# Performance work log

Measured on AMD Instinct MI355X. Metric: run time of the kernel, lower is better.

The kernel has to match this reference:

```python
import jax, jax.numpy as jnp
import numpy as np

B, S, C, D, H = 2, 2048, 512, 768, 12
DH = D // H
DFF = 3072
EPS = 1e-5
NEG = 10000.0


def _layernorm(x, g, b):
    mu = jnp.mean(x, axis=-1, keepdims=True)
    var = jnp.mean((x - mu) ** 2, axis=-1, keepdims=True)
    return (x - mu) / jnp.sqrt(var + EPS) * g + b


def setup_inputs() -> dict:
    key = jax.random.key(0)
    ks = jax.random.split(key, 8)
    std = 0.02
    return {
        "x": jax.random.normal(ks[0], (B, S, D), jnp.float32),
        "context_seq": jax.random.normal(ks[1], (B, C, D), jnp.float32),
        "ln1_g": jnp.ones((D,), jnp.float32),
        "ln1_b": jnp.zeros((D,), jnp.float32),
        "Wattn": std * jax.random.normal(ks[2], (D, 3 * D), jnp.float32),
        "battn": jnp.zeros((3 * D,), jnp.float32),
        "Wref": std * jax.random.normal(ks[3], (D, 2 * D), jnp.float32),
        "bref": jnp.zeros((2 * D,), jnp.float32),
        "Wproj": std * jax.random.normal(ks[4], (D, D), jnp.float32),
        "bproj": jnp.zeros((D,), jnp.float32),
        "ln2_g": jnp.ones((D,), jnp.float32),
        "ln2_b": jnp.zeros((D,), jnp.float32),
        "W1": std * jax.random.normal(ks[5], (D, DFF), jnp.float32),
        "b1": jnp.zeros((DFF,), jnp.float32),
        "W2": std * jax.random.normal(ks[6], (DFF, D), jnp.float32),
        "b2": jnp.zeros((D,), jnp.float32),
        "context_attn_bias": jnp.ones((), jnp.float32),
        "cs_self_attn_mask_prob": 1,
    }


def reference(x, context_seq, ln1_g, ln1_b, Wattn, battn, Wref, bref,
              Wproj, bproj, ln2_g, ln2_b, W1, b1, W2, b2,
              context_attn_bias, cs_self_attn_mask_prob):
    # --- CoconBlock: no history_seq -> history_seq_len = 0, offset = 0 ---
    h1 = _layernorm(x, ln1_g, ln1_b)

    # fused qkv (Conv1D == x @ W + b)
    qkv = h1 @ Wattn + battn
    q, k, v = jnp.split(qkv, 3, axis=-1)            # each [B,S,D]
    kv_ctx = context_seq @ Wref + bref
    kc, vc = jnp.split(kv_ctx, 2, axis=-1)          # each [B,C,D]

    kp = jnp.concatenate([kc, k], axis=1)           # [B,C+S,D]
    vp = jnp.concatenate([vc, v], axis=1)
    ns = C + S

    qh = q.reshape(B, S, H, DH)
    kh = kp.reshape(B, ns, H, DH)
    vh = vp.reshape(B, ns, H, DH)

    # scores (scale=False in original call path -> unscaled QK^T)
    w = jnp.einsum('bqhd,bkhd->bhqk', qh, kh)       # [B,H,S,ns]

    qi = jnp.arange(S)[:, None]
    kj = jnp.arange(ns)[None, :]
    # causal bias slice: tril rows ns-nd..ns-1 -> attend iff kj <= qi + C
    causal = (kj <= qi + C).astype(w.dtype)
    w = w * causal - NEG * (1.0 - causal)

    # self-token mask (cs_self_attn_mask_prob == 1: fully deterministic path;
    # history_seq_len = 0 -> offset 0 -> masks element (i, i))
    if cs_self_attn_mask_prob > 0:
        stm = (kj != qi).astype(w.dtype)
        w = w * stm - NEG * (1.0 - stm)

    # context attention bias on the first C key columns
    ctx_cols = (kj < C).astype(w.dtype)
    w = w + context_attn_bias * ctx_cols

    p = jax.nn.softmax(w, axis=-1)                  # attn_dropout: eval/identity
    a = jnp.einsum('bhqk,bkhd->bqhd', p, vh).reshape(B, S, D)
    a = a @ Wproj + bproj                           # resid_dropout: identity

    x1 = x + a                                      # history_seq_len <= 1: no slice
    h2 = _layernorm(x1, ln2_g, ln2_b)
    m = jax.nn.silu(h2 @ W1 + b1) @ W2 + b2
    out = x1 + m
    return out[:, 1:, :]                            # include_sos_output=False
```

## Files before the change

### kernel.cpp

```cpp
#include <hip/hip_runtime.h>
#include <hip/hip_bf16.h>
#include <math.h>

#define B_   2
#define S_   2048
#define C_   512
#define D_   768
#define H_   12
#define DH_  64
#define DFF_ 3072
#define NS_  (C_ + S_)

typedef __attribute__((ext_vector_type(8))) short          bf16x8;
typedef __attribute__((ext_vector_type(4))) float          f32x4;
typedef __attribute__((ext_vector_type(8))) unsigned short us8;
typedef __attribute__((ext_vector_type(4))) unsigned short us4;

static __device__ __forceinline__ unsigned short f2b(float f) {
    unsigned int u = __float_as_uint(f);
    unsigned int r = (u + 0x7FFFu + ((u >> 16) & 1u)) >> 16;
    return (unsigned short)r;
}
static __device__ __forceinline__ float b2f(unsigned short u) {
    return __uint_as_float(((unsigned int)u) << 16);
}

#define ASYNC_LDS16(gp, lp)                                                     \
    __builtin_amdgcn_global_load_lds(                                           \
        (const __attribute__((address_space(1))) void*)(gp),                    \
        (__attribute__((address_space(3))) void*)(lp), 16, 0, 0)

#define XCD_SWIZZLE_2D(MB, NB, TM, TN)                                          \
    int nwg_ = gridDim.x * gridDim.y;                                           \
    int bid_ = blockIdx.y * gridDim.x + blockIdx.x;                             \
    int q8_  = nwg_ >> 3;                                                       \
    int swz_ = (bid_ & 7) * q8_ + (bid_ >> 3);                                  \
    int MB = (swz_ / gridDim.x) * (TM);                                         \
    int NB = (swz_ % gridDim.x) * (TN);

__global__ __launch_bounds__(256) void ln_kernel(const float* __restrict__ in,
                                                 const float* __restrict__ g,
                                                 const float* __restrict__ bta,
                                                 unsigned short* __restrict__ out)
{
    int row = blockIdx.x;
    int tid = threadIdx.x;
    const float* x = in + (size_t)row * D_;
    float v0 = x[tid], v1 = x[tid + 256], v2 = x[tid + 512];
    float s  = v0 + v1 + v2;
    float s2 = v0 * v0 + v1 * v1 + v2 * v2;
#pragma unroll
    for (int off = 32; off >= 1; off >>= 1) {
        s  += __shfl_down(s,  off, 64);
        s2 += __shfl_down(s2, off, 64);
    }
    __shared__ float sh[8];
    int lane = tid & 63, wv = tid >> 6;
    if (lane == 0) { sh[wv] = s; sh[4 + wv] = s2; }
    __syncthreads();
    s  = sh[0] + sh[1] + sh[2] + sh[3];
    s2 = sh[4] + sh[5] + sh[6] + sh[7];
    float mu   = s * (1.0f / D_);
    float var  = s2 * (1.0f / D_) - mu * mu;
    float rstd = rsqrtf(var + 1e-5f);
    unsigned short* o = out + (size_t)row * D_;
    o[tid]       = f2b((v0 - mu) * rstd * g[tid]       + bta[tid]);
    o[tid + 256] = f2b((v1 - mu) * rstd * g[tid + 256] + bta[tid + 256]);
    o[tid + 512] = f2b((v2 - mu) * rstd * g[tid + 512] + bta[tid + 512]);
}

__global__ __launch_bounds__(256) void wprep(
    const float* __restrict__ Wattn, const float* __restrict__ Wref,
    const float* __restrict__ Wproj, const float* __restrict__ W1,
    const float* __restrict__ W2,    const float* __restrict__ ctx,
    unsigned short* __restrict__ wattnT, unsigned short* __restrict__ wrefT,
    unsigned short* __restrict__ wprojT, unsigned short* __restrict__ w1T,
    unsigned short* __restrict__ w2T,    unsigned short* __restrict__ ctxb)
{
    int bid = blockIdx.x;
    if (bid >= 8064) {
        int i = (bid - 8064) * 256 + threadIdx.x;
        float4 v = ((const float4*)ctx)[i];
        us4 o = { f2b(v.x), f2b(v.y), f2b(v.z), f2b(v.w) };
        ((us4*)ctxb)[i] = o;
        return;
    }
    const float* in; unsigned short* outp; int K, N, nt;
    if (bid < 1728)      {             in = Wattn; outp = wattnT; K = 768;  N = 2304; nt = 72; }
    else if (bid < 2880) { bid -= 1728; in = Wref;  outp = wrefT;  K = 768;  N = 1536; nt = 48; }
    else if (bid < 3456) { bid -= 2880; in = Wproj; outp = wprojT; K = 768;  N = 768;  nt = 24; }
    else if (bid < 5760) { bid -= 3456; in = W1;    outp = w1T;    K = 768;  N = 3072; nt = 96; }
    else                 { bid -= 5760; in = W2;    outp = w2T;    K = 3072; N = 768;  nt = 24; }
    int n0 = (bid % nt) * 32, k0 = (bid / nt) * 32;

    __shared__ float t[32][33];
    int tx = threadIdx.x & 31, ty = threadIdx.x >> 5;
#pragma unroll
    for (int i = 0; i < 32; i += 8)
        t[ty + i][tx] = in[(size_t)(k0 + ty + i) * N + n0 + tx];
    __syncthreads();
#pragma unroll
    for (int i = 0; i < 32; i += 8)
        outp[(size_t)(n0 + ty + i) * K + k0 + tx] = f2b(t[tx][ty + i]);
}

#define GEMM_EPI_ELEM()                                                         \
    {                                                                           \
        float v = accv[q] + bv;                                                 \
        if (ACT) v = v / (1.0f + __expf(-v));                                   \
        if (RESID) v += resid[(size_t)grow * N + gcol];                         \
        if (OUTBF) {                                                            \
            outb[(size_t)grow * N + gcol] = f2b(v);                             \
        } else if (SLICE) {                                                     \
            int bb = grow >> 11, ss = grow & 2047;                              \
            if (ss > 0)                                                         \
                outf[((size_t)(bb * 2047 + ss - 1)) * N + gcol] = v;            \
        } else {                                                                \
            outf[(size_t)grow * N + gcol] = v;                                  \
        }                                                                       \
    }

template <int ACT, int RESID, int SLICE, int OUTBF>
__global__ __launch_bounds__(256) void gemm_mfma(
    const unsigned short* __restrict__ A,
    const unsigned short* __restrict__ BT,
    const float* __restrict__ bias,
    const float* __restrict__ resid,
    float* __restrict__ outf,
    unsigned short* __restrict__ outb,
    int M, int N, int K)
{
    __shared__ unsigned short Als[128 * 64];
    __shared__ unsigned short Bls[128 * 64];

    int tid  = threadIdx.x;
    int lane = tid & 63, w = tid >> 6;
    XCD_SWIZZLE_2D(mb, nb, 128, 128)
    int wr = w >> 1, wc = w & 1;

    f32x4 acc[4][4];
#pragma unroll
    for (int m = 0; m < 4; ++m)
#pragma unroll
        for (int n = 0; n < 4; ++n)
            acc[m][n] = (f32x4){0.f, 0.f, 0.f, 0.f};

    int srow = w * 32 + (lane >> 3);
    int scol = (lane & 7) * 8;
    const unsigned short* abase = A  + (size_t)(mb + srow) * K + scol;
    const unsigned short* bbase = BT + (size_t)(nb + srow) * K + scol;

    int arow_l = wr * 64 + (lane & 15);
    int brow_l = wc * 64 + (lane & 15);
    int kfrag  = (lane >> 4) * 8;

    for (int kk = 0; kk < K; kk += 64) {
        __syncthreads();
#pragma unroll
        for (int i = 0; i < 4; ++i) {
            ASYNC_LDS16(abase + (size_t)(i * 8) * K + kk,
                        (char*)Als + (w * 32 + i * 8) * 128);
            ASYNC_LDS16(bbase + (size_t)(i * 8) * K + kk,
                        (char*)Bls + (w * 32 + i * 8) * 128);
        }
        __syncthreads();
#pragma unroll
        for (int ks = 0; ks < 64; ks += 32) {
            bf16x8 af[4], bq[4];
#pragma unroll
            for (int m = 0; m < 4; ++m)
                af[m] = *(const bf16x8*)&Als[(arow_l + m * 16) * 64 + ks + kfrag];
#pragma unroll
            for (int n = 0; n < 4; ++n)
                bq[n] = *(const bf16x8*)&Bls[(brow_l + n * 16) * 64 + ks + kfrag];
#pragma unroll
            for (int m = 0; m < 4; ++m)
#pragma unroll
                for (int n = 0; n < 4; ++n)
                    acc[m][n] = __builtin_amdgcn_mfma_f32_16x16x32_bf16(
                        af[m], bq[n], acc[m][n], 0, 0, 0);
        }
    }

#pragma unroll
    for (int m = 0; m < 4; ++m) {
        int grow0 = mb + wr * 64 + m * 16 + ((lane >> 4) << 2);
#pragma unroll
        for (int n = 0; n < 4; ++n) {
            int gcol = nb + wc * 64 + n * 16 + (lane & 15);
            float bv = bias[gcol];
#pragma unroll
            for (int q = 0; q < 4; ++q) {
                int grow = grow0 + q;
                float accv[4] = {acc[m][n][0], acc[m][n][1], acc[m][n][2], acc[m][n][3]};
                GEMM_EPI_ELEM()
            }
        }
    }
}

template <int ACT, int RESID, int SLICE, int OUTBF>
__global__ __launch_bounds__(256) void gemm_mfma64(
    const unsigned short* __restrict__ A,
    const unsigned short* __restrict__ BT,
    const float* __restrict__ bias,
    const float* __restrict__ resid,
    float* __restrict__ outf,
    unsigned short* __restrict__ outb,
    int M, int N, int K)
{
    __shared__ unsigned short Als[64 * 64];
    __shared__ unsigned short Bls[128 * 64];

    int tid  = threadIdx.x;
    int lane = tid & 63, w = tid >> 6;
    XCD_SWIZZLE_2D(mb, nb, 64, 128)

    f32x4 acc[4][2];
#pragma unroll
    for (int m = 0; m < 4; ++m)
#pragma unroll
        for (int n = 0; n < 2; ++n)
            acc[m][n] = (f32x4){0.f, 0.f, 0.f, 0.f};

    int srow = w * 8 + (lane >> 3);
    int scol = (lane & 7) * 8;
    const unsigned short* abase = A  + (size_t)(mb + srow) * K + scol;
    const unsigned short* bbase = BT + (size_t)(nb + srow) * K + scol;

    int arow_l = lane & 15;
    int brow_l = w * 32 + (lane & 15);
    int kfrag  = (lane >> 4) * 8;

    for (int kk = 0; kk < K; kk += 64) {
        __syncthreads();
#pragma unroll
        for (int i = 0; i < 2; ++i)
            ASYNC_LDS16(abase + (size_t)(i * 32) * K + kk,
                        (char*)Als + i * 4096 + w * 1024);
#pragma unroll
        for (int i = 0; i < 4; ++i)
            ASYNC_LDS16(bbase + (size_t)(i * 32) * K + kk,
                        (char*)Bls + i * 4096 + w * 1024);
        __syncthreads();
#pragma unroll
        for (int ks = 0; ks < 64; ks += 32) {
            bf16x8 af[4], bq[2];
#pragma unroll
            for (int m = 0; m < 4; ++m)
                af[m] = *(const bf16x8*)&Als[(arow_l + m * 16) * 64 + ks + kfrag];
#pragma unroll
            for (int n = 0; n < 2; ++n)
                bq[n] = *(const bf16x8*)&Bls[(brow_l + n * 16) * 64 + ks + kfrag];
#pragma unroll
            for (int m = 0; m < 4; ++m)
#pragma unroll
                for (int n = 0; n < 2; ++n)
                    acc[m][n] = __builtin_amdgcn_mfma_f32_16x16x32_bf16(
                        af[m], bq[n], acc[m][n], 0, 0, 0);
        }
    }

#pragma unroll
    for (int m = 0; m < 4; ++m) {
        int grow0 = mb + m * 16 + ((lane >> 4) << 2);
#pragma unroll
        for (int n = 0; n < 2; ++n) {
            int gcol = nb + w * 32 + n * 16 + (lane & 15);
            float bv = bias[gcol];
#pragma unroll
            for (int q = 0; q < 4; ++q) {
                int grow = grow0 + q;
                float accv[4] = {acc[m][n][0], acc[m][n][1], acc[m][n][2], acc[m][n][3]};
                GEMM_EPI_ELEM()
            }
        }
    }
}

__device__ const int ATT_QT[21] = {10,9,8,7,6,5,15,15,14, 4,14,13,13,12, 3,12,11,11, 2,1,0};
__device__ const int ATT_T0[21] = { 0,0,0,0,0,0, 0,10, 0, 0,10, 0, 9, 0, 0, 9, 0, 8, 0,0,0};
__device__ const int ATT_T1[21] = {15,14,13,12,11,10,10,20,10, 9,19, 9,18, 9, 8,17, 8,16, 7,6,5};

__global__ __launch_bounds__(512, 2) void attn_mfma(const unsigned short* __restrict__ qkv,
                                                    const unsigned short* __restrict__ kvctx,
                                                    const float* __restrict__ cabp,
                                                    const int* __restrict__ smpp,
                                                    unsigned short* __restrict__ aout,
                                                    float* __restrict__ Opart,
                                                    float* __restrict__ mlpart)
{
    __shared__ unsigned short Kls[128 * 64];
    __shared__ unsigned short Vt [64 * 136];
    __shared__ unsigned short Pls[128 * 136];

    int bid = blockIdx.x;
    int j = (bid < 256) ? bid : 503 - (bid - 256);
    int rank = j / 24, grp = j % 24;
    int h = grp % 12, b = grp / 12;
    int qt = ATT_QT[rank], t0 = ATT_T0[rank], t1 = ATT_T1[rank];
    bool split = (t1 - t0) < (qt + 5);
    int half = (t0 > 0) ? 1 : 0;

    int tid = threadIdx.x;
    int l = tid & 63, w = tid >> 6;
    int g = l >> 4, lc = l & 15;
    float cab = *cabp;
    int   smp = *smpp;
    int qbase = qt * 128;

    bf16x8 qf0, qf1;
    {
        const unsigned short* qp = qkv + ((size_t)(b * S_ + qbase + w * 16 + lc)) * (3 * D_)
                                       + h * DH_ + g * 8;
        qf0 = *(const bf16x8*)(qp);
        qf1 = *(const bf16x8*)(qp + 32);
    }

    f32x4 acc[4];
#pragma unroll
    for (int n = 0; n < 4; ++n) acc[n] = (f32x4){0.f, 0.f, 0.f, 0.f};
    float mrow[4], lrow[4];
#pragma unroll
    for (int e = 0; e < 4; ++e) { mrow[e] = -1e30f; lrow[e] = 0.f; }

    int colu = 8 * ((l & 7) ^ (l >> 3));
    int kvr  = tid >> 3;
    int d0   = (tid & 7) * 8;
    int dsw  = (tid & 7) << 3;
    int vtrow[8];
#pragma unroll
    for (int jj = 0; jj < 8; ++jj) vtrow[jj] = (d0 + jj) * 136;
    int vo0 = kvr ^ dsw, vo1 = (64 + kvr) ^ dsw;
    int ksw  = (lc & 7) << 3;
    int koff0 = (g * 8) ^ ksw, koff1 = (32 + g * 8) ^ ksw;
    us8 vr0, vr1;

#define STAGE_TILE(TT)                                                                   \
    {                                                                                    \
        int kb2 = (TT) * 128;                                                            \
        bool isctx = (kb2 < C_);                                                         \
        _Pragma("unroll")                                                                \
        for (int s2 = 0; s2 < 2; ++s2) {                                                 \
            int s = w * 2 + s2;                                                          \
            int kj = kb2 + s * 8 + (l >> 3);                                             \
            const unsigned short* src = isctx                                            \
                ? kvctx + ((size_t)(b * C_ + kj)) * (2 * D_) + h * DH_ + colu            \
                : qkv + ((size_t)(b * S_ + kj - C_)) * (3 * D_) + D_ + h * DH_ + colu;   \
            ASYNC_LDS16(src, (char*)Kls + s * 1024);                                     \
        }                                                                                \
        int kv0 = kb2 + kvr;                                                             \
        vr0 = *(const us8*)(isctx                                                        \
            ? kvctx + ((size_t)(b * C_ + kv0)) * (2 * D_) + D_ + h * DH_ + d0            \
            : qkv + ((size_t)(b * S_ + kv0 - C_)) * (3 * D_) + 2 * D_ + h * DH_ + d0);   \
        vr1 = *(const us8*)(isctx                                                        \
            ? kvctx + ((size_t)(b * C_ + kv0 + 64)) * (2 * D_) + D_ + h * DH_ + d0       \
            : qkv + ((size_t)(b * S_ + kv0 + 64 - C_)) * (3 * D_) + 2 * D_ + h * DH_ + d0); \
    }

    STAGE_TILE(t0)

    for (int t = t0; t < t1; ++t) {
        int kb = t * 128;
        __syncthreads();

#pragma unroll
        for (int jj = 0; jj < 8; ++jj) {
            Vt[vtrow[jj] + vo0] = vr0[jj];
            Vt[vtrow[jj] + vo1] = vr1[jj];
        }

        f32x4 s4[8];
#pragma unroll
        for (int nf = 0; nf < 8; ++nf) s4[nf] = (f32x4){0.f, 0.f, 0.f, 0.f};
        __builtin_amdgcn_s_setprio(1);
#pragma unroll
        for (int nf = 0; nf < 8; ++nf) {
            bf16x8 kf0 = *(const bf16x8*)&Kls[(nf * 16 + lc) * 64 + koff0];
            bf16x8 kf1 = *(const bf16x8*)&Kls[(nf * 16 + lc) * 64 + koff1];
            s4[nf] = __builtin_amdgcn_mfma_f32_16x16x32_bf16(qf0, kf0, s4[nf], 0, 0, 0);
            s4[nf] = __builtin_amdgcn_mfma_f32_16x16x32_bf16(qf1, kf1, s4[nf], 0, 0, 0);
        }
        __builtin_amdgcn_s_setprio(0);

        bool edge_t = (t == qt + 4);
        bool diag_t = (kb == qbase) && (smp > 0);
        float tb = (kb < C_) ? cab : 0.0f;

        if (edge_t) {
#pragma unroll
            for (int nf = 0; nf < 8; ++nf) {
                int kj = kb + nf * 16 + lc;
#pragma unroll
                for (int e = 0; e < 4; ++e) {
                    int qi = qbase + w * 16 + g * 4 + e;
                    s4[nf][e] = (kj <= qi + C_) ? s4[nf][e] : -10000.0f;
                }
            }
        }
        if (diag_t) {
#pragma unroll
            for (int nf = 0; nf < 8; ++nf) {
                int kj = kb + nf * 16 + lc;
#pragma unroll
                for (int e = 0; e < 4; ++e) {
                    int qi = qbase + w * 16 + g * 4 + e;
                    if (kj == qi) s4[nf][e] = -10000.0f;
                }
            }
        }

        float tmax[4], mbase[4], psum[4];
#pragma unroll
        for (int e = 0; e < 4; ++e) {
            float u0 = fmaxf(fmaxf(s4[0][e], s4[1][e]), fmaxf(s4[2][e], s4[3][e]));
            float u1 = fmaxf(fmaxf(s4[4][e], s4[5][e]), fmaxf(s4[6][e], s4[7][e]));
            tmax[e] = fmaxf(u0, u1);
        }
#pragma unroll
        for (int e = 0; e < 4; ++e) {
            tmax[e] = fmaxf(tmax[e], __shfl_xor(tmax[e], 1));
            tmax[e] = fmaxf(tmax[e], __shfl_xor(tmax[e], 2));
            tmax[e] = fmaxf(tmax[e], __shfl_xor(tmax[e], 4));
            tmax[e] = fmaxf(tmax[e], __shfl_xor(tmax[e], 8));
        }
#pragma unroll
        for (int e = 0; e < 4; ++e) {
            float mn = fmaxf(mrow[e], tmax[e] + tb);
            if (mn > mrow[e]) {
                float sc = __expf(mrow[e] - mn);
#pragma unroll
                for (int nf2 = 0; nf2 < 4; ++nf2) acc[nf2][e] *= sc;
                lrow[e] *= sc;
                mrow[e] = mn;
            }
            mbase[e] = mrow[e] - tb;
            psum[e] = 0.f;
        }
#pragma unroll
        for (int nf = 0; nf < 8; ++nf)
#pragma unroll
            for (int e = 0; e < 4; ++e) {
                float p = __expf(s4[nf][e] - mbase[e]);
                s4[nf][e] = p;
                psum[e] += p;
            }
#pragma unroll
        for (int e = 0; e < 4; ++e) lrow[e] += psum[e];

#pragma unroll
        for (int e = 0; e < 4; ++e) {
            int q = w * 16 + g * 4 + e;
            int qrow = q * 136, qsw = (q & 7) << 3;
#pragma unroll
            for (int a = 0; a < 4; ++a) {
                unsigned int pk;
                asm("v_cvt_pk_bf16_f32 %0, %1, %2"
                    : "=v"(pk) : "v"(s4[2 * a][e]), "v"(s4[2 * a + 1][e]));
                int xk = (a * 32 + lc) ^ qsw;
                Pls[qrow + xk]        = (unsigned short)pk;
                Pls[qrow + (xk ^ 16)] = (unsigned short)(pk >> 16);
            }
        }

        __syncthreads();

        if (t + 1 < t1) STAGE_TILE(t + 1)

        {
            int qa = w * 16 + lc;
            int qrow = qa * 136, qsw = (qa & 7) << 3;
            __builtin_amdgcn_s_setprio(1);
#pragma unroll
            for (int ks2 = 0; ks2 < 4; ++ks2) {
                bf16x8 pf = *(const bf16x8*)&Pls[qrow + ((ks2 * 32 + g * 8) ^ qsw)];
#pragma unroll
                for (int nf2 = 0; nf2 < 4; ++nf2) {
                    int d = nf2 * 16 + lc;
                    bf16x8 vf = *(const bf16x8*)&Vt[d * 136 +
                                   ((ks2 * 32 + g * 8) ^ (((d >> 3) & 7) << 3))];
                    acc[nf2] = __builtin_amdgcn_mfma_f32_16x16x32_bf16(pf, vf, acc[nf2], 0, 0, 0);
                }
            }
            __builtin_amdgcn_s_setprio(0);
        }
    }

#pragma unroll
    for (int e = 0; e < 4; ++e) {
        lrow[e] += __shfl_xor(lrow[e], 1);
        lrow[e] += __shfl_xor(lrow[e], 2);
        lrow[e] += __shfl_xor(lrow[e], 4);
        lrow[e] += __shfl_xor(lrow[e], 8);
    }
    if (!split) {
#pragma unroll
        for (int e = 0; e < 4; ++e) {
            int q = qbase + w * 16 + g * 4 + e;
            float inv = 1.0f / lrow[e];
            unsigned short* dst = &aout[((size_t)(b * S_ + q)) * D_ + h * DH_];
#pragma unroll
            for (int nf2 = 0; nf2 < 4; ++nf2)
                dst[nf2 * 16 + lc] = f2b(acc[nf2][e] * inv);
        }
    } else {
        int rec = ((b * 12 + h) * 5 + (qt - 11)) * 2 + half;
        float* Ob  = Opart + (size_t)rec * 8192;
        float* mlb = mlpart + rec * 256;
#pragma unroll
        for (int e = 0; e < 4; ++e) {
            int row = w * 16 + g * 4 + e;
#pragma unroll
            for (int nf2 = 0; nf2 < 4; ++nf2)
                Ob[row * 64 + nf2 * 16 + lc] = acc[nf2][e];
            if (lc == 0) { mlb[row * 2] = mrow[e]; mlb[row * 2 + 1] = lrow[e]; }
        }
    }
#undef STAGE_TILE
}

__global__ __launch_bounds__(256) void attn_merge(const float* __restrict__ Opart,
                                                  const float* __restrict__ mlpart,
                                                  unsigned short* __restrict__ aout)
{
    int rec = blockIdx.x;
    int qidx = rec % 5;
    int bh = rec / 5;
    int h = bh % 12, b = bh / 12;
    int qt = 11 + qidx;
    int row = threadIdx.x >> 1, dbase = (threadIdx.x & 1) * 32;

    const float* O0  = Opart + ((size_t)(rec * 2 + 0)) * 8192 + row * 64 + dbase;
    const float* O1  = Opart + ((size_t)(rec * 2 + 1)) * 8192 + row * 64 + dbase;
    const float* ml0 = mlpart + (rec * 2 + 0) * 256 + row * 2;
    const float* ml1 = mlpart + (rec * 2 + 1) * 256 + row * 2;
    float m0 = ml0[0], l0 = ml0[1];
    float m1 = ml1[0], l1 = ml1[1];
    float m  = fmaxf(m0, m1);
    float c0 = __expf(m0 - m), c1 = __expf(m1 - m);
    float inv = 1.0f / (l0 * c0 + l1 * c1);

    int q = qt * 128 + row;
    unsigned short* dst = &aout[((size_t)(b * S_ + q)) * D_ + h * DH_ + dbase];
#pragma unroll
    for (int jj = 0; jj < 32; ++jj)
        dst[jj] = f2b((O0[jj] * c0 + O1[jj] * c1) * inv);
}

extern "C" void kernel_launch(void* const* d_in, const int* in_sizes, int n_in,
                              void* d_out, int out_size, void* d_ws, size_t ws_size,
                              hipStream_t stream)
{
    const float* x     = (const float*)d_in[0];
    const float* ctx   = (const float*)d_in[1];
    const float* ln1g  = (const float*)d_in[2];
    const float* ln1b  = (const float*)d_in[3];
    const float* Wattn = (const float*)d_in[4];
    const float* battn = (const float*)d_in[5];
    const float* Wref  = (const float*)d_in[6];
    const float* bref  = (const float*)d_in[7];
    const float* Wproj = (const float*)d_in[8];
    const float* bproj = (const float*)d_in[9];
    const float* ln2g  = (const float*)d_in[10];
    const float* ln2b  = (const float*)d_in[11];
    const float* W1    = (const float*)d_in[12];
    const float* b1    = (const float*)d_in[13];
    const float* W2    = (const float*)d_in[14];
    const float* b2    = (const float*)d_in[15];
    const float* cab   = (const float*)d_in[16];
    const int*   smp   = (const int*)d_in[17];
    float* out = (float*)d_out;

    float* ws = (float*)d_ws;
    unsigned short* qkvb   = (unsigned short*)(ws + 0);
    unsigned short* ff1b   = (unsigned short*)(ws + 0);
    unsigned short* kvctxb = (unsigned short*)(ws + 4718592);
    unsigned short* attnb  = (unsigned short*)(ws + 5505024);
    unsigned short* hb     = (unsigned short*)(ws + 7077888);
    float*          x1     = ws + 8650752;
    float*          Opart  = ws + 7077888;
    float*          mlpart = ws + 11010048;
    unsigned short* ctxb   = (unsigned short*)(ws + 11796480);
    unsigned short* wts    = (unsigned short*)(ws + 12189696);
    unsigned short* wattnT = wts;
    unsigned short* wrefT  = wts + 1769472;
    unsigned short* wprojT = wts + 2949120;
    unsigned short* w1T    = wts + 3538944;
    unsigned short* w2T    = wts + 5898240;

    wprep<<<8832, 256, 0, stream>>>(Wattn, Wref, Wproj, W1, W2, ctx,
                                    wattnT, wrefT, wprojT, w1T, w2T, ctxb);

    ln_kernel<<<B_ * S_, 256, 0, stream>>>(x, ln1g, ln1b, hb);
    gemm_mfma<0, 0, 0, 1><<<dim3(18, 32), 256, 0, stream>>>(
        hb, wattnT, battn, nullptr, nullptr, qkvb, 4096, 2304, 768);
    gemm_mfma64<0, 0, 0, 1><<<dim3(12, 16), 256, 0, stream>>>(
        ctxb, wrefT, bref, nullptr, nullptr, kvctxb, 1024, 1536, 768);
    attn_mfma<<<504, 512, 0, stream>>>(qkvb, kvctxb, cab, smp, attnb, Opart, mlpart);
    attn_merge<<<120, 256, 0, stream>>>(Opart, mlpart, attnb);
    gemm_mfma64<0, 1, 0, 0><<<dim3(6, 64), 256, 0, stream>>>(
        attnb, wprojT, bproj, x, x1, nullptr, 4096, 768, 768);
    ln_kernel<<<B_ * S_, 256, 0, stream>>>(x1, ln2g, ln2b, hb);
    gemm_mfma<1, 0, 0, 1><<<dim3(24, 32), 256, 0, stream>>>(
        hb, w1T, b1, nullptr, nullptr, ff1b, 4096, 3072, 768);
    gemm_mfma64<0, 1, 1, 0><<<dim3(6, 64), 256, 0, stream>>>(
        ff1b, w2T, b2, x1, out, nullptr, 4096, 768, 3072);
}
```

Before: 276.8 us.

## Fuse LN1 into weight prep, merge QKV and context GEMMs, use exp2 softmax

Folds the first layernorm into the weight-prep launch as extra blocks and merges the QKV and context-KV projections into a single GEMM launch, removing two kernel launches and the tail idle time between them. The attention kernel now multiplies Q by log2(e) once at load, then uses exp2f in the online softmax and in the merge step, with the mask constants and context bias rescaled to match. The extra bf16 rounding of the prescaled Q slightly perturbs numerics, and the context GEMM now runs with 128-row tiles instead of the 64-row variant.

```diff
diff --git a/kernel.cpp b/kernel.cpp
--- a/kernel.cpp
+++ b/kernel.cpp
@@ -10,6 +10,7 @@
 #define DH_  64
 #define DFF_ 3072
 #define NS_  (C_ + S_)
+#define LOG2E_ 1.44269504f
 
 typedef __attribute__((ext_vector_type(8))) short          bf16x8;
 typedef __attribute__((ext_vector_type(4))) float          f32x4;
@@ -73,13 +74,45 @@
     const float* __restrict__ Wattn, const float* __restrict__ Wref,
     const float* __restrict__ Wproj, const float* __restrict__ W1,
     const float* __restrict__ W2,    const float* __restrict__ ctx,
+    const float* __restrict__ x,     const float* __restrict__ ln1g,
+    const float* __restrict__ ln1b,
     unsigned short* __restrict__ wattnT, unsigned short* __restrict__ wrefT,
     unsigned short* __restrict__ wprojT, unsigned short* __restrict__ w1T,
-    unsigned short* __restrict__ w2T,    unsigned short* __restrict__ ctxb)
+    unsigned short* __restrict__ w2T,    unsigned short* __restrict__ ctxb,
+    unsigned short* __restrict__ hb)
 {
+    __shared__ float t[32][33];
+    __shared__ float sh[8];
     int bid = blockIdx.x;
+    int tid = threadIdx.x;
+
+    if (bid >= 8832) {
+        int row = bid - 8832;
+        const float* xr = x + (size_t)row * D_;
+        float v0 = xr[tid], v1 = xr[tid + 256], v2 = xr[tid + 512];
+        float s  = v0 + v1 + v2;
+        float s2 = v0 * v0 + v1 * v1 + v2 * v2;
+#pragma unroll
+        for (int off = 32; off >= 1; off >>= 1) {
+            s  += __shfl_down(s,  off, 64);
+            s2 += __shfl_down(s2, off, 64);
+        }
+        int lane = tid & 63, wv = tid >> 6;
+        if (lane == 0) { sh[wv] = s; sh[4 + wv] = s2; }
+        __syncthreads();
+        s  = sh[0] + sh[1] + sh[2] + sh[3];
+        s2 = sh[4] + sh[5] + sh[6] + sh[7];
+        float mu   = s * (1.0f / D_);
+        float var  = s2 * (1.0f / D_) - mu * mu;
+        float rstd = rsqrtf(var + 1e-5f);
+        unsigned short* o = hb + (size_t)row * D_;
+        o[tid]       = f2b((v0 - mu) * rstd * ln1g[tid]       + ln1b[tid]);
+        o[tid + 256] = f2b((v1 - mu) * rstd * ln1g[tid + 256] + ln1b[tid + 256]);
+        o[tid + 512] = f2b((v2 - mu) * rstd * ln1g[tid + 512] + ln1b[tid + 512]);
+        return;
+    }
     if (bid >= 8064) {
-        int i = (bid - 8064) * 256 + threadIdx.x;
+        int i = (bid - 8064) * 256 + tid;
         float4 v = ((const float4*)ctx)[i];
         us4 o = { f2b(v.x), f2b(v.y), f2b(v.z), f2b(v.w) };
         ((us4*)ctxb)[i] = o;
@@ -92,9 +125,7 @@
     else if (bid < 5760) { bid -= 3456; in = W1;    outp = w1T;    K = 768;  N = 3072; nt = 96; }
     else                 { bid -= 5760; in = W2;    outp = w2T;    K = 3072; N = 768;  nt = 24; }
     int n0 = (bid % nt) * 32, k0 = (bid / nt) * 32;
-
-    __shared__ float t[32][33];
-    int tx = threadIdx.x & 31, ty = threadIdx.x >> 5;
+    int tx = tid & 31, ty = tid >> 5;
 #pragma unroll
     for (int i = 0; i < 32; i += 8)
         t[ty + i][tx] = in[(size_t)(k0 + ty + i) * N + n0 + tx];
@@ -120,6 +151,88 @@
         }                                                                       \
     }
 
+__global__ __launch_bounds__(256) void gemm_qkv_ctx(
+    const unsigned short* __restrict__ hb, const unsigned short* __restrict__ wattnT,
+    const float* __restrict__ battn, unsigned short* __restrict__ qkvb,
+    const unsigned short* __restrict__ ctxb, const unsigned short* __restrict__ wrefT,
+    const float* __restrict__ bref, unsigned short* __restrict__ kvctxb)
+{
+    __shared__ unsigned short Als[128 * 64];
+    __shared__ unsigned short Bls[128 * 64];
+
+    int bid = blockIdx.x;
+    const unsigned short *A, *BT; const float* bias; unsigned short* outb;
+    int N, gx, nblk, sb;
+    if (bid < 576) { A = hb;   BT = wattnT; bias = battn; outb = qkvb;   N = 2304; gx = 18; nblk = 576; sb = bid; }
+    else           { A = ctxb; BT = wrefT;  bias = bref;  outb = kvctxb; N = 1536; gx = 12; nblk = 96;  sb = bid - 576; }
+    int swz = (sb & 7) * (nblk >> 3) + (sb >> 3);
+    int mb = (swz / gx) * 128, nb = (swz % gx) * 128;
+    const int K = 768;
+
+    int tid  = threadIdx.x;
+    int lane = tid & 63, w = tid >> 6;
+    int wr = w >> 1, wc = w & 1;
+
+    f32x4 acc[4][4];
+#pragma unroll
+    for (int m = 0; m < 4; ++m)
+#pragma unroll
+        for (int n = 0; n < 4; ++n)
+            acc[m][n] = (f32x4){0.f, 0.f, 0.f, 0.f};
+
+    int srow = w * 32 + (lane >> 3);
+    int scol = (lane & 7) * 8;
+    const unsigned short* abase = A  + (size_t)(mb + srow) * K + scol;
+    const unsigned short* bbase = BT + (size_t)(nb + srow) * K + scol;
+
+    int arow_l = wr * 64 + (lane & 15);
+    int brow_l = wc * 64 + (lane & 15);
+    int kfrag  = (lane >> 4) * 8;
+
+    for (int kk = 0; kk < K; kk += 64) {
+        __syncthreads();
+#pragma unroll
+        for (int i = 0; i < 4; ++i) {
+            ASYNC_LDS16(abase + (size_t)(i * 8) * K + kk,
+                        (char*)Als + (w * 32 + i * 8) * 128);
+            ASYNC_LDS16(bbase + (size_t)(i * 8) * K + kk,
+                        (char*)Bls + (w * 32 + i * 8) * 128);
+        }
+        __syncthreads();
+#pragma unroll
+        for (int ks = 0; ks < 64; ks += 32) {
+            bf16x8 af[4], bq[4];
+#pragma unroll
+            for (int m = 0; m < 4; ++m)
+                af[m] = *(const bf16x8*)&Als[(arow_l + m * 16) * 64 + ks + kfrag];
+#pragma unroll
+            for (int n = 0; n < 4; ++n)
+                bq[n] = *(const bf16x8*)&Bls[(brow_l + n * 16) * 64 + ks + kfrag];
+#pragma unroll
+            for (int m = 0; m < 4; ++m)
+#pragma unroll
+                for (int n = 0; n < 4; ++n)
+                    acc[m][n] = __builtin_amdgcn_mfma_f32_16x16x32_bf16(
+                        af[m], bq[n], acc[m][n], 0, 0, 0);
+        }
+    }
+
+#pragma unroll
+    for (int m = 0; m < 4; ++m) {
+        int grow0 = mb + wr * 64 + m * 16 + ((lane >> 4) << 2);
+#pragma unroll
+        for (int n = 0; n < 4; ++n) {
+            int gcol = nb + wc * 64 + n * 16 + (lane & 15);
+            float bv = bias[gcol];
+#pragma unroll
+            for (int q = 0; q < 4; ++q) {
+                int grow = grow0 + q;
+                outb[(size_t)grow * N + gcol] = f2b(acc[m][n][q] + bv);
+            }
+        }
+    }
+}
+
 template <int ACT, int RESID, int SLICE, int OUTBF>
 __global__ __launch_bounds__(256) void gemm_mfma(
     const unsigned short* __restrict__ A,
@@ -315,6 +428,11 @@
                                        + h * DH_ + g * 8;
         qf0 = *(const bf16x8*)(qp);
         qf1 = *(const bf16x8*)(qp + 32);
+#pragma unroll
+        for (int i = 0; i < 8; ++i) {
+            qf0[i] = (short)f2b(b2f((unsigned short)qf0[i]) * LOG2E_);
+            qf1[i] = (short)f2b(b2f((unsigned short)qf1[i]) * LOG2E_);
+        }
     }
 
     f32x4 acc[4];
@@ -385,7 +503,7 @@
 
         bool edge_t = (t == qt + 4);
         bool diag_t = (kb == qbase) && (smp > 0);
-        float tb = (kb < C_) ? cab : 0.0f;
+        float tb = (kb < C_) ? cab * LOG2E_ : 0.0f;
 
         if (edge_t) {
 #pragma unroll
@@ -394,7 +512,7 @@
 #pragma unroll
                 for (int e = 0; e < 4; ++e) {
                     int qi = qbase + w * 16 + g * 4 + e;
-                    s4[nf][e] = (kj <= qi + C_) ? s4[nf][e] : -10000.0f;
+                    s4[nf][e] = (kj <= qi + C_) ? s4[nf][e] : -100000.0f;
                 }
             }
         }
@@ -405,7 +523,7 @@
 #pragma unroll
                 for (int e = 0; e < 4; ++e) {
                     int qi = qbase + w * 16 + g * 4 + e;
-                    if (kj == qi) s4[nf][e] = -10000.0f;
+                    if (kj == qi) s4[nf][e] = -100000.0f;
                 }
             }
         }
@@ -428,7 +546,7 @@
         for (int e = 0; e < 4; ++e) {
             float mn = fmaxf(mrow[e], tmax[e] + tb);
             if (mn > mrow[e]) {
-                float sc = __expf(mrow[e] - mn);
+                float sc = exp2f(mrow[e] - mn);
 #pragma unroll
                 for (int nf2 = 0; nf2 < 4; ++nf2) acc[nf2][e] *= sc;
                 lrow[e] *= sc;
@@ -441,7 +559,7 @@
         for (int nf = 0; nf < 8; ++nf)
 #pragma unroll
             for (int e = 0; e < 4; ++e) {
-                float p = __expf(s4[nf][e] - mbase[e]);
+                float p = exp2f(s4[nf][e] - mbase[e]);
                 s4[nf][e] = p;
                 psum[e] += p;
             }
@@ -537,7 +655,7 @@
     float m0 = ml0[0], l0 = ml0[1];
     float m1 = ml1[0], l1 = ml1[1];
     float m  = fmaxf(m0, m1);
-    float c0 = __expf(m0 - m), c1 = __expf(m1 - m);
+    float c0 = exp2f(m0 - m), c1 = exp2f(m1 - m);
     float inv = 1.0f / (l0 * c0 + l1 * c1);
 
     int q = qt * 128 + row;
@@ -588,14 +706,10 @@
     unsigned short* w1T    = wts + 3538944;
     unsigned short* w2T    = wts + 5898240;
 
-    wprep<<<8832, 256, 0, stream>>>(Wattn, Wref, Wproj, W1, W2, ctx,
-                                    wattnT, wrefT, wprojT, w1T, w2T, ctxb);
-
-    ln_kernel<<<B_ * S_, 256, 0, stream>>>(x, ln1g, ln1b, hb);
-    gemm_mfma<0, 0, 0, 1><<<dim3(18, 32), 256, 0, stream>>>(
-        hb, wattnT, battn, nullptr, nullptr, qkvb, 4096, 2304, 768);
-    gemm_mfma64<0, 0, 0, 1><<<dim3(12, 16), 256, 0, stream>>>(
-        ctxb, wrefT, bref, nullptr, nullptr, kvctxb, 1024, 1536, 768);
+    wprep<<<12928, 256, 0, stream>>>(Wattn, Wref, Wproj, W1, W2, ctx, x, ln1g, ln1b,
+                                     wattnT, wrefT, wprojT, w1T, w2T, ctxb, hb);
+    gemm_qkv_ctx<<<672, 256, 0, stream>>>(hb, wattnT, battn, qkvb,
+                                          ctxb, wrefT, bref, kvctxb);
     attn_mfma<<<504, 512, 0, stream>>>(qkvb, kvctxb, cab, smp, attnb, Opart, mlpart);
     attn_merge<<<120, 256, 0, stream>>>(Opart, mlpart, attnb);
     gemm_mfma64<0, 1, 0, 0><<<dim3(6, 64), 256, 0, stream>>>(
```

New measurement: 272.2 us. Within noise of the previous version (-1.6%).
